# Performance work log

Hardware: AMD Instinct MI355X
Metric: run time of the kernel (lower is better)

The kernel has to match this reference:

```python
import jax, jax.numpy as jnp
import numpy as np

N_NODES = 50000
N_EDGES = 800000
IN_CH = 128
HID_CH = 256  # 2 * out_channels
OUT_CH = 128


def setup_inputs() -> dict:
    key = jax.random.key(0)
    ks = jax.random.split(key, 8)
    x = jax.random.normal(ks[0], (N_NODES, IN_CH), dtype=jnp.float32)
    edge_index = jax.random.randint(ks[1], (2, N_EDGES), 0, N_NODES, dtype=jnp.int64)
    batch = jnp.zeros((N_NODES,), dtype=jnp.int64)
    # GCNConv weights (PyG: glorot init; here random normal scaled)
    W1 = jax.random.normal(ks[2], (IN_CH, HID_CH), dtype=jnp.float32) / np.sqrt(IN_CH)
    b1 = jnp.zeros((HID_CH,), dtype=jnp.float32)
    W2 = jax.random.normal(ks[3], (HID_CH, OUT_CH), dtype=jnp.float32) / np.sqrt(HID_CH)
    b2 = jnp.zeros((OUT_CH,), dtype=jnp.float32)
    return {"x": x, "edge_index": edge_index, "batch": batch,
            "W1": W1, "b1": b1, "W2": W2, "b2": b2}


def _gcn_norm(edge_index, num_nodes):
    # add self-loops, compute symmetric normalization (PyG GCNConv default)
    loop = jnp.arange(num_nodes, dtype=edge_index.dtype)
    src = jnp.concatenate([edge_index[0], loop])
    dst = jnp.concatenate([edge_index[1], loop])
    deg = jax.ops.segment_sum(jnp.ones_like(dst, dtype=jnp.float32), dst,
                              num_segments=num_nodes)
    dis = jnp.where(deg > 0, jax.lax.rsqrt(deg), 0.0)  # deg^{-1/2}, inf->0
    norm = dis[src] * dis[dst]  # [E+N]
    return src, dst, norm


def _gcn_conv(x, W, b, src, dst, norm, num_nodes):
    h = x @ W                              # [N, F_out] dense GEMM
    msg = h[src] * norm[:, None]           # gather + per-edge scale
    out = jax.ops.segment_sum(msg, dst, num_segments=num_nodes)  # scatter-add
    return out + b


def reference(x, edge_index, batch, W1, b1, W2, b2):
    n = x.shape[0]
    src, dst, norm = _gcn_norm(edge_index, n)
    h = jax.nn.relu(_gcn_conv(x, W1, b1, src, dst, norm, n))
    h = jax.nn.relu(_gcn_conv(h, W2, b2, src, dst, norm, n))
    return h
```

## Files before the change

### kernel.cpp

```cpp
#include <hip/hip_runtime.h>

#define N_NODES 50000
#define N_EDGES 800000
#define IN_CH 128
#define HID_CH 256
#define OUT_CH 128

constexpr int TOTAL_E = N_EDGES + N_NODES;
constexpr int NBKT = 196;
constexpr int NBLK_BIN = 128;
constexpr int EPB_BIN = N_EDGES / NBLK_BIN;
constexpr int CNT2D = NBKT * NBLK_BIN;
constexpr int SCAN_BLK = 1024;
constexpr int NB_SC = (CNT2D + SCAN_BLK - 1) / SCAN_BLK;
constexpr int COLCAP = 5376;

typedef __attribute__((ext_vector_type(8))) short bf16x8;
typedef __attribute__((ext_vector_type(4))) float f32x4;
typedef __attribute__((ext_vector_type(4))) unsigned int u32x4;


__device__ __forceinline__ unsigned int bf16rn(float x) {
    unsigned int u = __float_as_uint(x);
    return (u + 0x7fffu + ((u >> 16) & 1u)) >> 16;
}

__device__ __forceinline__ void split2(float x0, float x1,
                                       unsigned int& h, unsigned int& l) {
    unsigned int h0 = bf16rn(x0), h1 = bf16rn(x1);
    float f0 = __uint_as_float(h0 << 16), f1 = __uint_as_float(h1 << 16);
    unsigned int l0 = bf16rn(x0 - f0), l1 = bf16rn(x1 - f1);
    h = h0 | (h1 << 16);
    l = l0 | (l1 << 16);
}

__device__ __forceinline__ bf16x8 asbf(u32x4 v) {
    return __builtin_bit_cast(bf16x8, v);
}


__global__ void k_tobf(const float* __restrict__ x, unsigned short* __restrict__ xb,
                       int n8) {
    int i = blockIdx.x * blockDim.x + threadIdx.x;
    if (i >= n8) return;
    const float4* p = (const float4*)(x + (size_t)i * 8);
    float4 a = p[0], b = p[1];
    u32x4 w;
    w.x = bf16rn(a.x) | (bf16rn(a.y) << 16);
    w.y = bf16rn(a.z) | (bf16rn(a.w) << 16);
    w.z = bf16rn(b.x) | (bf16rn(b.y) << 16);
    w.w = bf16rn(b.z) | (bf16rn(b.w) << 16);
    *(u32x4*)(xb + (size_t)i * 8) = w;
}


__global__ __launch_bounds__(256)
void k_count(const int* __restrict__ dst, int* __restrict__ cnt2D) {
    __shared__ int h[NBKT];
    int b = blockIdx.x, t = threadIdx.x;
    if (t < NBKT) h[t] = 0;
    __syncthreads();
    int e0 = b * EPB_BIN;
    for (int i = t; i < EPB_BIN; i += 256)
        atomicAdd(&h[dst[e0 + i] >> 8], 1);
    __syncthreads();
    if (t < NBKT) cnt2D[t * NBLK_BIN + b] = h[t];
}

__global__ void k_scan1(const int* __restrict__ cnt, int* __restrict__ incl,
                        int* __restrict__ part, int n) {
    __shared__ int s[SCAN_BLK];
    int t = threadIdx.x;
    int i = blockIdx.x * SCAN_BLK + t;
    int v = (i < n) ? cnt[i] : 0;
    s[t] = v; __syncthreads();
    for (int o = 1; o < SCAN_BLK; o <<= 1) {
        int a = (t >= o) ? s[t - o] : 0;
        __syncthreads();
        s[t] += a;
        __syncthreads();
    }
    if (i < n) incl[i] = s[t];
    if (t == SCAN_BLK - 1) part[blockIdx.x] = s[t];
}

__global__ void k_scan2(int* __restrict__ part, int n) {
    __shared__ int s[SCAN_BLK];
    int t = threadIdx.x;
    int v = (t < n) ? part[t] : 0;
    s[t] = v; __syncthreads();
    for (int o = 1; o < SCAN_BLK; o <<= 1) {
        int a = (t >= o) ? s[t - o] : 0;
        __syncthreads();
        s[t] += a;
        __syncthreads();
    }
    if (t < n) part[t] = s[t] - v;
}

__global__ void k_off(int* __restrict__ incl, const int* __restrict__ cnt,
                      const int* __restrict__ part, int n, int total) {
    int i = blockIdx.x * blockDim.x + threadIdx.x;
    if (i < n)       incl[i] = part[i >> 10] + incl[i] - cnt[i];
    else if (i == n) incl[i] = total;
}

__global__ __launch_bounds__(256)
void k_bin(const int* __restrict__ src, const int* __restrict__ dst,
           const int* __restrict__ off2D, int2* __restrict__ binned) {
    __shared__ int cur[NBKT];
    int b = blockIdx.x, t = threadIdx.x;
    if (t < NBKT) cur[t] = off2D[t * NBLK_BIN + b];
    __syncthreads();
    int e0 = b * EPB_BIN;
    for (int i = t; i < EPB_BIN; i += 256) {
        int d = dst[e0 + i];
        int pos = atomicAdd(&cur[d >> 8], 1);
        int2 p; p.x = src[e0 + i]; p.y = d;
        binned[pos] = p;
    }
}

__global__ __launch_bounds__(256)
void k_csr(const int2* __restrict__ binned, const int* __restrict__ off2D,
           int* __restrict__ col, int* __restrict__ off, float* __restrict__ dis) {
    __shared__ int cnt[256], sc[256], cur[256];
    __shared__ int colL[COLCAP];
    int kb = blockIdx.x, t = threadIdx.x;
    int base2 = off2D[kb * NBLK_BIN];
    int end2  = off2D[(kb + 1) * NBLK_BIN];
    int nE = end2 - base2;
    int nn = min(256, N_NODES - kb * 256);
    cnt[t] = 0;
    __syncthreads();
    for (int i = t; i < nE; i += 256)
        atomicAdd(&cnt[binned[base2 + i].y & 255], 1);
    __syncthreads();
    sc[t] = cnt[t];
    __syncthreads();
    for (int o = 1; o < 256; o <<= 1) {
        int a = (t >= o) ? sc[t - o] : 0;
        __syncthreads();
        sc[t] += a;
        __syncthreads();
    }
    int excl = sc[t] - cnt[t];
    cur[t] = excl + t;
    __syncthreads();
    for (int i = t; i < nE; i += 256) {
        int2 p = binned[base2 + i];
        colL[atomicAdd(&cur[p.y & 255], 1)] = p.x;
    }
    __syncthreads();
    int v = kb * 256 + t;
    if (t < nn) {
        colL[cur[t]] = v;
        off[v] = base2 + kb * 256 + excl + t;
        dis[v] = rsqrtf((float)(cnt[t] + 1));
    }
    if (kb == NBKT - 1 && t == 0) off[N_NODES] = TOTAL_E;
    __syncthreads();
    int tot = nE + nn, gbase = base2 + kb * 256;
    for (int i = t; i < tot; i += 256)
        col[gbase + i] = colL[i];
}


template<bool BIAS, bool RELU, bool BF16OUT>
__global__ __launch_bounds__(256)
void k_agg_bf(const unsigned short* __restrict__ featb, const int* __restrict__ col,
              const int* __restrict__ off, const float* __restrict__ dis,
              const float* __restrict__ bias, void* __restrict__ outv) {
    int wid  = threadIdx.x >> 6;
    int lane = threadIdx.x & 63;
    int v = blockIdx.x * 4 + wid;
    int start = off[v];
    int lenv  = off[v + 1] - start;
    float disv = dis[v];
    int half = lane >> 5;
    int q    = lane & 31;
    float4 acc = make_float4(0.f, 0.f, 0.f, 0.f);
    for (int base = 0; base < lenv; base += 64) {
        int n = min(64, lenv - base);
        int   cv = 0;
        float wv = 0.f;
        if (lane < n) {
            cv = col[start + base + lane];
            wv = dis[cv] * disv;
        }
        auto pair = [&](int j) {
            int   c = __shfl(cv, j + half);
            float w = __shfl(wv, j + half);
            uint2 d = *(const uint2*)&featb[(size_t)c * 128 + q * 4];
            acc.x = fmaf(w, __uint_as_float(d.x << 16),         acc.x);
            acc.y = fmaf(w, __uint_as_float(d.x & 0xffff0000u), acc.y);
            acc.z = fmaf(w, __uint_as_float(d.y << 16),         acc.z);
            acc.w = fmaf(w, __uint_as_float(d.y & 0xffff0000u), acc.w);
        };
        int j = 0;
        for (; j + 8 <= n; j += 8) { pair(j); pair(j + 2); pair(j + 4); pair(j + 6); }
        for (; j < n; j += 2) pair(j);
    }
    acc.x += __shfl_xor(acc.x, 32);
    acc.y += __shfl_xor(acc.y, 32);
    acc.z += __shfl_xor(acc.z, 32);
    acc.w += __shfl_xor(acc.w, 32);
    if (half == 0) {
        float4 o = acc;
        if (BIAS) {
            float4 b = *(const float4*)&bias[q * 4];
            o.x += b.x; o.y += b.y; o.z += b.z; o.w += b.w;
        }
        if (RELU) {
            o.x = fmaxf(o.x, 0.f); o.y = fmaxf(o.y, 0.f);
            o.z = fmaxf(o.z, 0.f); o.w = fmaxf(o.w, 0.f);
        }
        if (BF16OUT) {
            uint2 p;
            p.x = bf16rn(o.x) | (bf16rn(o.y) << 16);
            p.y = bf16rn(o.z) | (bf16rn(o.w) << 16);
            *(uint2*)&((unsigned short*)outv)[(size_t)v * 128 + q * 4] = p;
        } else {
            *(float4*)&((float*)outv)[(size_t)v * 128 + q * 4] = o;
        }
    }
}


template<int K, int NC>
__device__ __forceinline__ void wsplit_body(const float* __restrict__ W,
                                            u32x4* __restrict__ Wf, int tid) {
    constexpr int NT = NC / 16;
    int lane = tid & 63;
    int ntk  = tid >> 6;
    int kt = ntk / NT, nt = ntk % NT;
    int kb = kt * 32 + (lane >> 4) * 8;
    int n  = nt * 16 + (lane & 15);
    unsigned int hh[4], ll[4];
    #pragma unroll
    for (int j = 0; j < 4; ++j) {
        float x0 = W[(size_t)(kb + 2 * j) * NC + n];
        float x1 = W[(size_t)(kb + 2 * j + 1) * NC + n];
        split2(x0, x1, hh[j], ll[j]);
    }
    Wf[(size_t)(ntk * 2 + 0) * 64 + lane] = (u32x4){hh[0], hh[1], hh[2], hh[3]};
    Wf[(size_t)(ntk * 2 + 1) * 64 + lane] = (u32x4){ll[0], ll[1], ll[2], ll[3]};
}

__global__ void k_wsplit_both(const float* __restrict__ W1, u32x4* __restrict__ Wf1,
                              const float* __restrict__ W2, u32x4* __restrict__ Wf2) {
    int tid = blockIdx.x * blockDim.x + threadIdx.x;
    if (tid < 4096)      wsplit_body<IN_CH,  HID_CH>(W1, Wf1, tid);
    else if (tid < 8192) wsplit_body<HID_CH, OUT_CH>(W2, Wf2, tid - 4096);
}


__global__ __launch_bounds__(256)
void k_gemm_fused(const unsigned short* __restrict__ Ab, const u32x4* __restrict__ Wf1,
                  const float* __restrict__ b1, const u32x4* __restrict__ Wf2,
                  unsigned short* __restrict__ outb, int M) {
    __shared__ unsigned short hh[32 * 256];
    int lane = threadIdx.x & 63, wid = threadIdx.x >> 6;
    int lq = lane >> 4, lr = lane & 15, kq = lq * 8;
    int rbase = blockIdx.x * 32;

    f32x4 acc[2][4];
    #pragma unroll
    for (int s = 0; s < 2; ++s)
        #pragma unroll
        for (int t = 0; t < 4; ++t) acc[s][t] = (f32x4){0.f, 0.f, 0.f, 0.f};

    for (int kt = 0; kt < 4; ++kt) {
        bf16x8 ah[2];
        #pragma unroll
        for (int s = 0; s < 2; ++s) {
            int row = min(rbase + s * 16 + lr, M - 1);
            ah[s] = *(const bf16x8*)&Ab[(size_t)row * IN_CH + kt * 32 + kq];
        }
        #pragma unroll
        for (int t = 0; t < 4; ++t) {
            int nt = wid * 4 + t;
            const u32x4* wp = Wf1 + (size_t)((kt * 16 + nt) * 2) * 64 + lane;
            bf16x8 bh = asbf(wp[0]);
            bf16x8 bl = asbf(wp[64]);
            acc[0][t] = __builtin_amdgcn_mfma_f32_16x16x32_bf16(ah[0], bh, acc[0][t], 0, 0, 0);
            acc[1][t] = __builtin_amdgcn_mfma_f32_16x16x32_bf16(ah[1], bh, acc[1][t], 0, 0, 0);
            acc[0][t] = __builtin_amdgcn_mfma_f32_16x16x32_bf16(ah[0], bl, acc[0][t], 0, 0, 0);
            acc[1][t] = __builtin_amdgcn_mfma_f32_16x16x32_bf16(ah[1], bl, acc[1][t], 0, 0, 0);
        }
    }

    #pragma unroll
    for (int t = 0; t < 4; ++t) {
        int colg = (wid * 4 + t) * 16 + lr;
        float bv = b1[colg];
        #pragma unroll
        for (int s = 0; s < 2; ++s) {
            #pragma unroll
            for (int j = 0; j < 4; ++j) {
                int row = s * 16 + lq * 4 + j;
                float o = fmaxf(acc[s][t][j] + bv, 0.f);
                int e = (row * 256 + colg) ^ ((row & 7) << 3);
                hh[e] = (unsigned short)bf16rn(o);
            }
        }
    }
    __syncthreads();

    f32x4 acc2[2][2];
    #pragma unroll
    for (int s = 0; s < 2; ++s)
        #pragma unroll
        for (int t = 0; t < 2; ++t) acc2[s][t] = (f32x4){0.f, 0.f, 0.f, 0.f};

    for (int kt = 0; kt < 8; ++kt) {
        bf16x8 ah[2];
        #pragma unroll
        for (int s = 0; s < 2; ++s) {
            int row = s * 16 + lr;
            int e = (row * 256 + kt * 32 + kq) ^ ((row & 7) << 3);
            ah[s] = *(const bf16x8*)&hh[e];
        }
        #pragma unroll
        for (int t = 0; t < 2; ++t) {
            int nt = wid * 2 + t;
            const u32x4* wp = Wf2 + (size_t)((kt * 8 + nt) * 2) * 64 + lane;
            bf16x8 bh = asbf(wp[0]);
            bf16x8 bl = asbf(wp[64]);
            acc2[0][t] = __builtin_amdgcn_mfma_f32_16x16x32_bf16(ah[0], bh, acc2[0][t], 0, 0, 0);
            acc2[1][t] = __builtin_amdgcn_mfma_f32_16x16x32_bf16(ah[1], bh, acc2[1][t], 0, 0, 0);
            acc2[0][t] = __builtin_amdgcn_mfma_f32_16x16x32_bf16(ah[0], bl, acc2[0][t], 0, 0, 0);
            acc2[1][t] = __builtin_amdgcn_mfma_f32_16x16x32_bf16(ah[1], bl, acc2[1][t], 0, 0, 0);
        }
    }

    #pragma unroll
    for (int t = 0; t < 2; ++t) {
        int colg = (wid * 2 + t) * 16 + lr;
        #pragma unroll
        for (int s = 0; s < 2; ++s) {
            #pragma unroll
            for (int j = 0; j < 4; ++j) {
                int row = rbase + s * 16 + lq * 4 + j;
                if (row < M)
                    outb[(size_t)row * OUT_CH + colg] =
                        (unsigned short)bf16rn(acc2[s][t][j]);
            }
        }
    }
}


extern "C" void kernel_launch(void* const* d_in, const int* in_sizes, int n_in,
                              void* d_out, int out_size, void* d_ws, size_t ws_size,
                              hipStream_t stream) {
    const float* x   = (const float*)d_in[0];
    const int*   ei  = (const int*)d_in[1];
    const int*   src = ei;
    const int*   dst = ei + N_EDGES;
    const float* W1  = (const float*)d_in[3];
    const float* b1  = (const float*)d_in[4];
    const float* W2  = (const float*)d_in[5];
    const float* b2  = (const float*)d_in[6];
    float* out = (float*)d_out;

    char* ws = (char*)d_ws;
    size_t o = 0;
    auto carve = [&](size_t bytes) {
        void* p = ws + o;
        o += (bytes + 255) & ~(size_t)255;
        return p;
    };
    int*   cnt2D  = (int*)  carve((size_t)CNT2D * 4);
    int*   incl2D = (int*)  carve((size_t)(CNT2D + 1) * 4);
    int*   part   = (int*)  carve(SCAN_BLK * 4);
    int*   off    = (int*)  carve((size_t)(N_NODES + 1) * 4);
    float* dis    = (float*)carve(N_NODES * 4);
    int*   col    = (int*)  carve((size_t)TOTAL_E * 4);
    char*  buf1   = (char*) carve((size_t)N_NODES * 128 * 2);
    unsigned short* bfbuf = (unsigned short*)carve((size_t)N_NODES * 128 * 2);
    u32x4* Wf1    = (u32x4*)carve((size_t)4 * 16 * 2 * 64 * 16);
    u32x4* Wf2    = (u32x4*)carve((size_t)8 * 8 * 2 * 64 * 16);
    int*   off2D  = incl2D;
    int2*           binned = (int2*)buf1;
    unsigned short* agg1b  = (unsigned short*)buf1;
    unsigned short* xb     = bfbuf;
    unsigned short* t2b    = bfbuf;

    const int B = 256;
    k_tobf  <<<(N_NODES * 128 / 8 + B - 1) / B, B, 0, stream>>>(x, xb, N_NODES * 128 / 8);
    k_count <<<NBLK_BIN, 256, 0, stream>>>(dst, cnt2D);
    k_scan1 <<<NB_SC, SCAN_BLK, 0, stream>>>(cnt2D, incl2D, part, CNT2D);
    k_scan2 <<<1, SCAN_BLK, 0, stream>>>(part, NB_SC);
    k_off   <<<(CNT2D + 1 + B - 1) / B, B, 0, stream>>>(incl2D, cnt2D, part, CNT2D, N_EDGES);
    k_bin   <<<NBLK_BIN, 256, 0, stream>>>(src, dst, off2D, binned);
    k_csr   <<<NBKT, 256, 0, stream>>>(binned, off2D, col, off, dis);
    k_wsplit_both<<<32, 256, 0, stream>>>(W1, Wf1, W2, Wf2);

    k_agg_bf<false, false, true><<<N_NODES / 4, 256, 0, stream>>>(
        xb, col, off, dis, nullptr, agg1b);
    k_gemm_fused<<<(N_NODES + 31) / 32, 256, 0, stream>>>(agg1b, Wf1, b1, Wf2, t2b, N_NODES);
    k_agg_bf<true, true, false><<<N_NODES / 4, 256, 0, stream>>>(
        t2b, col, off, dis, b2, out);
}
```

Baseline: 150.9 us.

## Fuse three-kernel scan into one block; widen aggregation to 16-byte loads, 4 edges per wave

Replaces the three-kernel scan (scan1, scan2, offset fixup) with a single 1024-thread block that scans per-thread chunks serially and then does one shared-memory scan, which cuts two launches. The aggregation kernel now has each group of 16 lanes load a full 256-byte bf16 row with 16-byte loads, so four edges are processed per wave step instead of two. It then reduces the partial sums across the four edge groups with two xor shuffles. This raises memory-level parallelism and load width but uses more accumulator registers and an extra reduction step.

```diff
diff --git a/kernel.cpp b/kernel.cpp
--- a/kernel.cpp
+++ b/kernel.cpp
@@ -11,8 +11,7 @@
 constexpr int NBLK_BIN = 128;
 constexpr int EPB_BIN = N_EDGES / NBLK_BIN;
 constexpr int CNT2D = NBKT * NBLK_BIN;
-constexpr int SCAN_BLK = 1024;
-constexpr int NB_SC = (CNT2D + SCAN_BLK - 1) / SCAN_BLK;
+constexpr int SCHUNK = (CNT2D + 1023) / 1024;
 constexpr int COLCAP = 5376;
 
 typedef __attribute__((ext_vector_type(8))) short bf16x8;
@@ -67,42 +66,34 @@
     if (t < NBKT) cnt2D[t * NBLK_BIN + b] = h[t];
 }
 
-__global__ void k_scan1(const int* __restrict__ cnt, int* __restrict__ incl,
-                        int* __restrict__ part, int n) {
-    __shared__ int s[SCAN_BLK];
+__global__ __launch_bounds__(1024)
+void k_scanall(const int* __restrict__ cnt, int* __restrict__ offo) {
+    __shared__ int s[1024];
     int t = threadIdx.x;
-    int i = blockIdx.x * SCAN_BLK + t;
-    int v = (i < n) ? cnt[i] : 0;
-    s[t] = v; __syncthreads();
-    for (int o = 1; o < SCAN_BLK; o <<= 1) {
+    int i0 = t * SCHUNK;
+    int loc[SCHUNK];
+    int sum = 0;
+    #pragma unroll
+    for (int k = 0; k < SCHUNK; ++k) {
+        int i = i0 + k;
+        int vv = (i < CNT2D) ? cnt[i] : 0;
+        loc[k] = sum;
+        sum += vv;
+    }
+    s[t] = sum; __syncthreads();
+    for (int o = 1; o < 1024; o <<= 1) {
         int a = (t >= o) ? s[t - o] : 0;
         __syncthreads();
         s[t] += a;
         __syncthreads();
     }
-    if (i < n) incl[i] = s[t];
-    if (t == SCAN_BLK - 1) part[blockIdx.x] = s[t];
-}
-
-__global__ void k_scan2(int* __restrict__ part, int n) {
-    __shared__ int s[SCAN_BLK];
-    int t = threadIdx.x;
-    int v = (t < n) ? part[t] : 0;
-    s[t] = v; __syncthreads();
-    for (int o = 1; o < SCAN_BLK; o <<= 1) {
-        int a = (t >= o) ? s[t - o] : 0;
-        __syncthreads();
-        s[t] += a;
-        __syncthreads();
-    }
-    if (t < n) part[t] = s[t] - v;
-}
-
-__global__ void k_off(int* __restrict__ incl, const int* __restrict__ cnt,
-                      const int* __restrict__ part, int n, int total) {
-    int i = blockIdx.x * blockDim.x + threadIdx.x;
-    if (i < n)       incl[i] = part[i >> 10] + incl[i] - cnt[i];
-    else if (i == n) incl[i] = total;
+    int base = s[t] - sum;
+    #pragma unroll
+    for (int k = 0; k < SCHUNK; ++k) {
+        int i = i0 + k;
+        if (i < CNT2D) offo[i] = base + loc[k];
+    }
+    if (t == 0) offo[CNT2D] = N_EDGES;
 }
 
 __global__ __launch_bounds__(256)
@@ -168,18 +159,18 @@
 
 template<bool BIAS, bool RELU, bool BF16OUT>
 __global__ __launch_bounds__(256)
-void k_agg_bf(const unsigned short* __restrict__ featb, const int* __restrict__ col,
-              const int* __restrict__ off, const float* __restrict__ dis,
-              const float* __restrict__ bias, void* __restrict__ outv) {
+void k_agg4(const unsigned short* __restrict__ featb, const int* __restrict__ col,
+            const int* __restrict__ off, const float* __restrict__ dis,
+            const float* __restrict__ bias, void* __restrict__ outv) {
     int wid  = threadIdx.x >> 6;
     int lane = threadIdx.x & 63;
     int v = blockIdx.x * 4 + wid;
     int start = off[v];
     int lenv  = off[v + 1] - start;
     float disv = dis[v];
-    int half = lane >> 5;
-    int q    = lane & 31;
-    float4 acc = make_float4(0.f, 0.f, 0.f, 0.f);
+    int eg = lane >> 4;
+    int h  = lane & 15;
+    float acc[8] = {0.f, 0.f, 0.f, 0.f, 0.f, 0.f, 0.f, 0.f};
     for (int base = 0; base < lenv; base += 64) {
         int n = min(64, lenv - base);
         int   cv = 0;
@@ -188,40 +179,48 @@
             cv = col[start + base + lane];
             wv = dis[cv] * disv;
         }
-        auto pair = [&](int j) {
-            int   c = __shfl(cv, j + half);
-            float w = __shfl(wv, j + half);
-            uint2 d = *(const uint2*)&featb[(size_t)c * 128 + q * 4];
-            acc.x = fmaf(w, __uint_as_float(d.x << 16),         acc.x);
-            acc.y = fmaf(w, __uint_as_float(d.x & 0xffff0000u), acc.y);
-            acc.z = fmaf(w, __uint_as_float(d.y << 16),         acc.z);
-            acc.w = fmaf(w, __uint_as_float(d.y & 0xffff0000u), acc.w);
+        auto step = [&](int j) {
+            int   c = __shfl(cv, j + eg);
+            float w = __shfl(wv, j + eg);
+            uint4 d = *(const uint4*)&featb[(size_t)c * 128 + h * 8];
+            acc[0] = fmaf(w, __uint_as_float(d.x << 16),         acc[0]);
+            acc[1] = fmaf(w, __uint_as_float(d.x & 0xffff0000u), acc[1]);
+            acc[2] = fmaf(w, __uint_as_float(d.y << 16),         acc[2]);
+            acc[3] = fmaf(w, __uint_as_float(d.y & 0xffff0000u), acc[3]);
+            acc[4] = fmaf(w, __uint_as_float(d.z << 16),         acc[4]);
+            acc[5] = fmaf(w, __uint_as_float(d.z & 0xffff0000u), acc[5]);
+            acc[6] = fmaf(w, __uint_as_float(d.w << 16),         acc[6]);
+            acc[7] = fmaf(w, __uint_as_float(d.w & 0xffff0000u), acc[7]);
         };
         int j = 0;
-        for (; j + 8 <= n; j += 8) { pair(j); pair(j + 2); pair(j + 4); pair(j + 6); }
-        for (; j < n; j += 2) pair(j);
-    }
-    acc.x += __shfl_xor(acc.x, 32);
-    acc.y += __shfl_xor(acc.y, 32);
-    acc.z += __shfl_xor(acc.z, 32);
-    acc.w += __shfl_xor(acc.w, 32);
-    if (half == 0) {
-        float4 o = acc;
+        for (; j + 16 <= n; j += 16) { step(j); step(j + 4); step(j + 8); step(j + 12); }
+        for (; j < n; j += 4) step(j);
+    }
+    #pragma unroll
+    for (int k = 0; k < 8; ++k) {
+        acc[k] += __shfl_xor(acc[k], 16);
+        acc[k] += __shfl_xor(acc[k], 32);
+    }
+    if (eg == 0) {
         if (BIAS) {
-            float4 b = *(const float4*)&bias[q * 4];
-            o.x += b.x; o.y += b.y; o.z += b.z; o.w += b.w;
+            #pragma unroll
+            for (int k = 0; k < 8; ++k) acc[k] += bias[h * 8 + k];
         }
         if (RELU) {
-            o.x = fmaxf(o.x, 0.f); o.y = fmaxf(o.y, 0.f);
-            o.z = fmaxf(o.z, 0.f); o.w = fmaxf(o.w, 0.f);
+            #pragma unroll
+            for (int k = 0; k < 8; ++k) acc[k] = fmaxf(acc[k], 0.f);
         }
         if (BF16OUT) {
-            uint2 p;
-            p.x = bf16rn(o.x) | (bf16rn(o.y) << 16);
-            p.y = bf16rn(o.z) | (bf16rn(o.w) << 16);
-            *(uint2*)&((unsigned short*)outv)[(size_t)v * 128 + q * 4] = p;
+            u32x4 p;
+            p.x = bf16rn(acc[0]) | (bf16rn(acc[1]) << 16);
+            p.y = bf16rn(acc[2]) | (bf16rn(acc[3]) << 16);
+            p.z = bf16rn(acc[4]) | (bf16rn(acc[5]) << 16);
+            p.w = bf16rn(acc[6]) | (bf16rn(acc[7]) << 16);
+            *(u32x4*)&((unsigned short*)outv)[(size_t)v * 128 + h * 8] = p;
         } else {
-            *(float4*)&((float*)outv)[(size_t)v * 128 + q * 4] = o;
+            float* op = (float*)outv + (size_t)v * 128 + h * 8;
+            *(float4*)op       = make_float4(acc[0], acc[1], acc[2], acc[3]);
+            *(float4*)(op + 4) = make_float4(acc[4], acc[5], acc[6], acc[7]);
         }
     }
 }
@@ -372,8 +371,7 @@
         return p;
     };
     int*   cnt2D  = (int*)  carve((size_t)CNT2D * 4);
-    int*   incl2D = (int*)  carve((size_t)(CNT2D + 1) * 4);
-    int*   part   = (int*)  carve(SCAN_BLK * 4);
+    int*   off2D  = (int*)  carve((size_t)(CNT2D + 1) * 4);
     int*   off    = (int*)  carve((size_t)(N_NODES + 1) * 4);
     float* dis    = (float*)carve(N_NODES * 4);
     int*   col    = (int*)  carve((size_t)TOTAL_E * 4);
@@ -381,25 +379,22 @@
     unsigned short* bfbuf = (unsigned short*)carve((size_t)N_NODES * 128 * 2);
     u32x4* Wf1    = (u32x4*)carve((size_t)4 * 16 * 2 * 64 * 16);
     u32x4* Wf2    = (u32x4*)carve((size_t)8 * 8 * 2 * 64 * 16);
-    int*   off2D  = incl2D;
     int2*           binned = (int2*)buf1;
     unsigned short* agg1b  = (unsigned short*)buf1;
     unsigned short* xb     = bfbuf;
     unsigned short* t2b    = bfbuf;
 
     const int B = 256;
-    k_tobf  <<<(N_NODES * 128 / 8 + B - 1) / B, B, 0, stream>>>(x, xb, N_NODES * 128 / 8);
-    k_count <<<NBLK_BIN, 256, 0, stream>>>(dst, cnt2D);
-    k_scan1 <<<NB_SC, SCAN_BLK, 0, stream>>>(cnt2D, incl2D, part, CNT2D);
-    k_scan2 <<<1, SCAN_BLK, 0, stream>>>(part, NB_SC);
-    k_off   <<<(CNT2D + 1 + B - 1) / B, B, 0, stream>>>(incl2D, cnt2D, part, CNT2D, N_EDGES);
-    k_bin   <<<NBLK_BIN, 256, 0, stream>>>(src, dst, off2D, binned);
-    k_csr   <<<NBKT, 256, 0, stream>>>(binned, off2D, col, off, dis);
+    k_tobf    <<<(N_NODES * 128 / 8 + B - 1) / B, B, 0, stream>>>(x, xb, N_NODES * 128 / 8);
+    k_count   <<<NBLK_BIN, 256, 0, stream>>>(dst, cnt2D);
+    k_scanall <<<1, 1024, 0, stream>>>(cnt2D, off2D);
+    k_bin     <<<NBLK_BIN, 256, 0, stream>>>(src, dst, off2D, binned);
+    k_csr     <<<NBKT, 256, 0, stream>>>(binned, off2D, col, off, dis);
     k_wsplit_both<<<32, 256, 0, stream>>>(W1, Wf1, W2, Wf2);
 
-    k_agg_bf<false, false, true><<<N_NODES / 4, 256, 0, stream>>>(
+    k_agg4<false, false, true><<<N_NODES / 4, 256, 0, stream>>>(
         xb, col, off, dis, nullptr, agg1b);
     k_gemm_fused<<<(N_NODES + 31) / 32, 256, 0, stream>>>(agg1b, Wf1, b1, Wf2, t2b, N_NODES);
-    k_agg_bf<true, true, false><<<N_NODES / 4, 256, 0, stream>>>(
+    k_agg4<true, true, false><<<N_NODES / 4, 256, 0, stream>>>(
         t2b, col, off, dis, b2, out);
 }
```

After: 162.2 us. +7.5%, slower.
